# Kernel tuning notes

Measured on AMD Instinct MI355X. Metric: run time of the kernel, lower is better.

Reference implementation:

```python
import jax, jax.numpy as jnp
import numpy as np

B, C, ROWS, COLS = 16, 1, 128, 128
E, H, L, VOCAB = 64, 32, 3, 258


def setup_inputs() -> dict:
    key = jax.random.key(0)
    ks = jax.random.split(key, 18)
    s = 0.05
    d = {
        "x": jax.random.randint(ks[0], (B, C, ROWS, COLS), 0, VOCAB, dtype=jnp.int32),
        "embed_table": jax.random.normal(ks[1], (VOCAB, E), jnp.float32) * s,
    }
    in_sizes = [E + 1, H, H]
    k = 2
    for l in range(L):
        d[f"w_ih_l{l}"] = jax.random.normal(ks[k], (3 * H, in_sizes[l]), jnp.float32) * s; k += 1
        d[f"w_hh_l{l}"] = jax.random.normal(ks[k], (3 * H, H), jnp.float32) * s; k += 1
        d[f"b_ih_l{l}"] = jax.random.normal(ks[k], (3 * H,), jnp.float32) * s; k += 1
        d[f"b_hh_l{l}"] = jax.random.normal(ks[k], (3 * H,), jnp.float32) * s; k += 1
    d["w_h2e"] = jax.random.normal(ks[14], (E + 1, H), jnp.float32) * s
    d["b_h2e"] = jax.random.normal(ks[15], (E + 1,), jnp.float32) * s
    d["w_out"] = jax.random.normal(ks[16], (VOCAB, H), jnp.float32) * s
    d["b_out"] = jax.random.normal(ks[17], (VOCAB,), jnp.float32) * s
    return d


def _forward(x, embed_table, wih, whh, bih, bhh, w_h2e, b_h2e, w_out, b_out):
    b, c, rows, cols = x.shape
    T = cols * c  # GRU sequence length per row
    Hh = whh[0].shape[1]
    nL = len(wih)

    xf = x.reshape(b, rows, T)
    emb = embed_table[xf]  # [B, rows, T, E]
    # normalized row coordinate in [-1, 1), appended as extra feature
    row_pos = jnp.arange(rows, dtype=emb.dtype) / rows * 2.0 - 1.0
    row_feat = jnp.broadcast_to(row_pos[None, :, None, None], (b, rows, T, 1))
    xin = jnp.concatenate([emb, row_feat], axis=-1)  # [B, rows, T, E+1]

    def gru_step(h, x_t):
        # h: [L, B, H]; x_t: [B, E+1]. torch GRU gate order: r, z, n.
        inp = x_t
        hs = []
        for l in range(nL):
            gi = inp @ wih[l].T + bih[l]
            gh = h[l] @ whh[l].T + bhh[l]
            ir, iz, inn = jnp.split(gi, 3, axis=-1)
            hr, hz, hn = jnp.split(gh, 3, axis=-1)
            r = jax.nn.sigmoid(ir + hr)
            z = jax.nn.sigmoid(iz + hz)
            n = jnp.tanh(inn + r * hn)
            hl = (1.0 - z) * n + z * h[l]
            hs.append(hl)
            inp = hl
        return jnp.stack(hs), inp  # emit top-layer output

    def row_step(prev_out, x_row):
        # prev_out: [B, T, H] top-layer GRU output of previous row
        comb = x_row + prev_out @ w_h2e.T + b_h2e  # [B, T, E+1]
        h0 = jnp.zeros((nL, b, Hh), comb.dtype)  # fresh h0 per row, as in torch
        _, out = jax.lax.scan(gru_step, h0, jnp.swapaxes(comb, 0, 1))  # [T, B, H]
        out = jnp.swapaxes(out, 0, 1)  # [B, T, H]
        return out, out

    prev0 = jnp.zeros((b, T, Hh), xin.dtype)
    _, outs = jax.lax.scan(row_step, prev0, jnp.swapaxes(xin, 0, 1))  # [rows, B, T, H]
    outs = jnp.swapaxes(outs, 0, 1)  # [B, rows, T, H]
    pred = outs @ w_out.T + b_out  # [B, rows, T, 258]
    return pred.reshape(b, c, rows, cols, VOCAB)


def reference(x, embed_table, w_ih_l0, w_hh_l0, b_ih_l0, b_hh_l0,
              w_ih_l1, w_hh_l1, b_ih_l1, b_hh_l1,
              w_ih_l2, w_hh_l2, b_ih_l2, b_hh_l2,
              w_h2e, b_h2e, w_out, b_out):
    return _forward(x, embed_table,
                    (w_ih_l0, w_ih_l1, w_ih_l2),
                    (w_hh_l0, w_hh_l1, w_hh_l2),
                    (b_ih_l0, b_ih_l1, b_ih_l2),
                    (b_hh_l0, b_hh_l1, b_hh_l2),
                    w_h2e, b_h2e, w_out, b_out)
```

## Files before the change

kernel.cpp:

```cpp
#include <hip/hip_runtime.h>
#include <math.h>

#define BATCH 16
#define RWS   128
#define TT    128
#define HH    32
#define GG    96
#define RPB   8
#define NRG   (RWS/RPB)
#define WP    100
#define FSTR  16

#define H2_BYTES   (BATCH*RWS*TT*HH*4)
#define FLAG_OFF   H2_BYTES
#define FLAG_BYTES (NRG*BATCH*FSTR*4)
#define PTAB_OFF   (FLAG_OFF + FLAG_BYTES)
#define WF_OFF     (PTAB_OFF + 258*GG*4)

__device__ __forceinline__ float sigm(float x) { return 1.0f / (1.0f + __expf(-x)); }
__device__ __forceinline__ float tanhfast(float x) {
  x = fminf(fmaxf(x, -15.0f), 15.0f);
  float e = __expf(2.0f * x);
  return (e - 1.0f) / (e + 1.0f);
}

__device__ __forceinline__ void barrier_lgkm() {
  __builtin_amdgcn_sched_barrier(0);
  asm volatile("s_waitcnt lgkmcnt(0)" ::: "memory");
  __builtin_amdgcn_s_barrier();
  __builtin_amdgcn_sched_barrier(0);
}

__device__ __forceinline__ float dot32p(const float4* __restrict__ w, const float4 v[8]) {
  float a0 = 0.f, a1 = 0.f, a2 = 0.f, a3 = 0.f;
#pragma unroll
  for (int c = 0; c < 8; ++c) {
    float4 W = w[c];
    a0 = fmaf(W.x, v[c].x, a0);
    a1 = fmaf(W.y, v[c].y, a1);
    a2 = fmaf(W.z, v[c].z, a2);
    a3 = fmaf(W.w, v[c].w, a3);
  }
  return (a0 + a1) + (a2 + a3);
}

__device__ __forceinline__ void hoist8(float4 dst[8], const float* __restrict__ src) {
  const float4* p = (const float4*)src;
#pragma unroll
  for (int c = 0; c < 8; ++c) dst[c] = p[c];
}

__global__ __launch_bounds__(128)
void prep_kernel(const float* __restrict__ emb, const float* __restrict__ wih0,
                 const float* __restrict__ bih0, const float* __restrict__ wh2e,
                 const float* __restrict__ bh2e, float* __restrict__ Ptab,
                 float* __restrict__ Wfo) {
  const int blk = blockIdx.x, tid = threadIdx.x;
  if (blk < 258) {
    if (tid < GG) {
      const float* wr = wih0 + tid * 65;
      const float* e  = emb + blk * 64;
      float acc = bih0[tid];
      for (int k = 0; k < 64; ++k) acc = fmaf(wr[k], e[k], acc);
      for (int k = 0; k < 65; ++k) acc = fmaf(wr[k], bh2e[k], acc);
      Ptab[blk * GG + tid] = acc;
    }
  } else {
    const int g = blk - 258;
    if (tid < HH) {
      const float* wr = wih0 + g * 65;
      float acc = 0.f;
      for (int k = 0; k < 65; ++k) acc = fmaf(wr[k], wh2e[k * HH + tid], acc);
      Wfo[g * HH + tid] = acc;
    }
  }
}

__device__ __forceinline__ void loadmat_packed(const float* __restrict__ src,
                                               float* __restrict__ dst, int tid) {
  for (int i = tid; i < GG * HH; i += 256) {
    const int g = i >> 5, k = i & 31;
    const int gate = g >> 5, j = g & 31;
    dst[j * WP + gate * 32 + k] = src[g * 32 + k];
  }
}

__global__ __launch_bounds__(256, 1)
void rnn_kernel(const int* __restrict__ xg, const float* __restrict__ wih0,
                const float* __restrict__ whh0g, const float* __restrict__ bhh0g,
                const float* __restrict__ wih1g, const float* __restrict__ whh1g,
                const float* __restrict__ bih1g, const float* __restrict__ bhh1g,
                const float* __restrict__ wih2g, const float* __restrict__ whh2g,
                const float* __restrict__ bih2g, const float* __restrict__ bhh2g,
                const float* __restrict__ Ptab, const float* __restrict__ Wfg,
                float* __restrict__ h2buf, int* __restrict__ flags) {
  extern __shared__ __align__(16) float lds[];
  float* Wf    = lds;
  float* Whh0  = Wf   + HH * WP;
  float* Wih1  = Whh0 + HH * WP;
  float* Whh1  = Wih1 + HH * WP;
  float* Wih2  = Whh1 + HH * WP;
  float* Whh2  = Wih2 + HH * WP;
  float* prevs = Whh2 + HH * WP;
  float* h0s   = prevs + HH;
  float* h1s   = h0s + RPB * HH;
  float* h2a   = h1s + RPB * HH;
  float* h2b   = h2a + RPB * HH;

  const int tid = threadIdx.x;
  const int j   = tid & 31;
  const int s   = tid >> 5;
  const int g   = blockIdx.x >> 4;
  const int bat = blockIdx.x & 15;
  const int row = g * RPB + s;

  loadmat_packed(Wfg,   Wf,   tid);
  loadmat_packed(whh0g, Whh0, tid);
  loadmat_packed(wih1g, Wih1, tid);
  loadmat_packed(whh1g, Whh1, tid);
  loadmat_packed(wih2g, Wih2, tid);
  loadmat_packed(whh2g, Whh2, tid);
  h0s[tid] = 0.f; h1s[tid] = 0.f; h2a[tid] = 0.f; h2b[tid] = 0.f;
  if (tid < HH) prevs[tid] = 0.f;

  const float bh0r = bhh0g[j], bh0z = bhh0g[32 + j], bh0n = bhh0g[64 + j];
  const float bi1r = bih1g[j], bi1z = bih1g[32 + j], bi1n = bih1g[64 + j];
  const float bh1r = bhh1g[j], bh1z = bhh1g[32 + j], bh1n = bhh1g[64 + j];
  const float bi2r = bih2g[j], bi2z = bih2g[32 + j], bi2n = bih2g[64 + j];
  const float bh2r_ = bhh2g[j], bh2z_ = bhh2g[32 + j], bh2n_ = bhh2g[64 + j];
  const float rowpos = (float)row * (2.0f / 128.0f) - 1.0f;
  const float rpr = wih0[j * 65 + 64] * rowpos;
  const float rpz = wih0[(32 + j) * 65 + 64] * rowpos;
  const float rpn = wih0[(64 + j) * 65 + 64] * rowpos;
  __syncthreads();

  float h0r = 0.f, h1r = 0.f, h2r = 0.f;
  float4 Vh0[8], Vh1[8], Vh2[8], Vp[8];
#pragma unroll
  for (int c = 0; c < 8; ++c) {
    Vh0[c] = make_float4(0.f, 0.f, 0.f, 0.f);
    Vh1[c] = make_float4(0.f, 0.f, 0.f, 0.f);
    Vh2[c] = make_float4(0.f, 0.f, 0.f, 0.f);
  }

  const size_t xbase = (size_t)(bat * RWS + row) * TT;
  const size_t obase = (size_t)(bat * RWS + row) * TT * HH + j;
  const size_t pbase = (row > 0) ? ((size_t)(bat * RWS + (row - 1)) * TT * HH + j) : 0;
  int* myflag = flags + (g * BATCH + bat) * FSTR;
  const int* pflag = flags + ((g > 0 ? g - 1 : 0) * BATCH + bat) * FSTR;

  int vcur = xg[xbase];
  float pvq = 0.f;
  int lastF = 0;

  if (g > 0) {
    if (tid == 0) {
      int f;
      do { f = __hip_atomic_load(pflag, __ATOMIC_RELAXED, __HIP_MEMORY_SCOPE_AGENT); }
      while (f < 1);
      lastF = f;
    }
    __syncthreads();
    if (s == 0)
      pvq = __hip_atomic_load(h2buf + pbase, __ATOMIC_RELAXED, __HIP_MEMORY_SCOPE_AGENT);
  }

  for (int i = 0; i < TT + RPB - 1; ++i) {
    const int t = i - s;
    const bool act = (t >= 0) && (t < TT);
    const float* h2rd = (i & 1) ? h2a : h2b;
    float*       h2w  = (i & 1) ? h2b : h2a;

    if (tid == 224 && i >= RPB) {
      asm volatile("s_waitcnt vmcnt(0)" ::: "memory");
      __hip_atomic_store(myflag, i - (RPB - 1), __ATOMIC_RELAXED, __HIP_MEMORY_SCOPE_AGENT);
    }

    const int tn = t + 1;
    const int vnext = (tn >= 0 && tn < TT) ? xg[xbase + tn] : 0;
    const float Pr = Ptab[vcur * GG + j];
    const float Pz = Ptab[vcur * GG + 32 + j];
    const float Pn = Ptab[vcur * GG + 64 + j];

    if (g > 0 && i < TT - 1) {
      if (tid == 0 && lastF < i + 2) {
        int f;
        do { f = __hip_atomic_load(pflag, __ATOMIC_RELAXED, __HIP_MEMORY_SCOPE_AGENT); }
        while (f < i + 2);
        lastF = f;
      }
    }
    barrier_lgkm();

    if (s == 0 && g > 0) {
      if (act) prevs[j] = pvq;
      if (i + 1 < TT)
        pvq = __hip_atomic_load(h2buf + pbase + (size_t)(i + 1) * HH,
                                __ATOMIC_RELAXED, __HIP_MEMORY_SCOPE_AGENT);
    }

    if (act) {
      const float ghr0 = bh0r + dot32p((const float4*)(Whh0 + j * WP),      Vh0);
      const float ghz0 = bh0z + dot32p((const float4*)(Whh0 + j * WP + 32), Vh0);
      const float ghn0 = bh0n + dot32p((const float4*)(Whh0 + j * WP + 64), Vh0);
      const float ghr1 = bh1r + dot32p((const float4*)(Whh1 + j * WP),      Vh1);
      const float ghz1 = bh1z + dot32p((const float4*)(Whh1 + j * WP + 32), Vh1);
      const float ghn1 = bh1n + dot32p((const float4*)(Whh1 + j * WP + 64), Vh1);
      const float ghr2 = bh2r_ + dot32p((const float4*)(Whh2 + j * WP),      Vh2);
      const float ghz2 = bh2z_ + dot32p((const float4*)(Whh2 + j * WP + 32), Vh2);
      const float ghn2 = bh2n_ + dot32p((const float4*)(Whh2 + j * WP + 64), Vh2);

      hoist8(Vp, (s == 0) ? prevs : (h2rd + (s - 1) * HH));
      {
        const float gir = Pr + rpr + dot32p((const float4*)(Wf + j * WP),      Vp);
        const float giz = Pz + rpz + dot32p((const float4*)(Wf + j * WP + 32), Vp);
        const float gin = Pn + rpn + dot32p((const float4*)(Wf + j * WP + 64), Vp);
        const float rg = sigm(gir + ghr0);
        const float zg = sigm(giz + ghz0);
        const float ng = tanhfast(gin + rg * ghn0);
        h0r = (1.f - zg) * ng + zg * h0r;
      }
      h0s[s * HH + j] = h0r;
      hoist8(Vh0, h0s + s * HH);

      {
        const float gir = bi1r + dot32p((const float4*)(Wih1 + j * WP),      Vh0);
        const float giz = bi1z + dot32p((const float4*)(Wih1 + j * WP + 32), Vh0);
        const float gin = bi1n + dot32p((const float4*)(Wih1 + j * WP + 64), Vh0);
        const float rg = sigm(gir + ghr1);
        const float zg = sigm(giz + ghz1);
        const float ng = tanhfast(gin + rg * ghn1);
        h1r = (1.f - zg) * ng + zg * h1r;
      }
      h1s[s * HH + j] = h1r;
      hoist8(Vh1, h1s + s * HH);

      {
        const float gir = bi2r + dot32p((const float4*)(Wih2 + j * WP),      Vh1);
        const float giz = bi2z + dot32p((const float4*)(Wih2 + j * WP + 32), Vh1);
        const float gin = bi2n + dot32p((const float4*)(Wih2 + j * WP + 64), Vh1);
        const float rg = sigm(gir + ghr2);
        const float zg = sigm(giz + ghz2);
        const float ng = tanhfast(gin + rg * ghn2);
        h2r = (1.f - zg) * ng + zg * h2r;
      }
      h2w[s * HH + j] = h2r;
      hoist8(Vh2, h2w + s * HH);

      if (s == RPB - 1) {
        __hip_atomic_store(h2buf + obase + (size_t)t * HH, h2r,
                           __ATOMIC_RELAXED, __HIP_MEMORY_SCOPE_AGENT);
      } else {
        h2buf[obase + (size_t)t * HH] = h2r;
      }
    }

    vcur = vnext;
  }

  if (tid == 224) {
    asm volatile("s_waitcnt vmcnt(0)" ::: "memory");
    __hip_atomic_store(myflag, TT, __ATOMIC_RELAXED, __HIP_MEMORY_SCOPE_AGENT);
  }
}

__global__ __launch_bounds__(256)
void proj_kernel(const float* __restrict__ h2buf, const float* __restrict__ wout,
                 const float* __restrict__ bout, float* __restrict__ out) {
  __shared__ float stage[32 * 258];
  const int tid = threadIdx.x;
  const int p = tid & 31, vq = tid >> 5;
  const size_t pos = (size_t)blockIdx.x * 32 + p;
  const float* hrow = h2buf + pos * HH;
  float h[HH];
#pragma unroll
  for (int k = 0; k < HH; k += 4) {
    float4 f = *(const float4*)(hrow + k);
    h[k] = f.x; h[k + 1] = f.y; h[k + 2] = f.z; h[k + 3] = f.w;
  }
#pragma unroll 1
  for (int vi = 0; vi <= 32; ++vi) {
    int v = vq + vi * 8;
    if (v < 258) {
      const float* wrow = wout + v * HH;
      float a0 = bout[v], a1 = 0.f;
#pragma unroll
      for (int k = 0; k < HH; k += 4) {
        float4 w = *(const float4*)(wrow + k);
        a0 = fmaf(w.x, h[k],     fmaf(w.y, h[k + 1], a0));
        a1 = fmaf(w.z, h[k + 2], fmaf(w.w, h[k + 3], a1));
      }
      stage[p * 258 + v] = a0 + a1;
    }
  }
  __syncthreads();
  float* o = out + (size_t)blockIdx.x * 32 * 258;
#pragma unroll 1
  for (int i = tid; i < 32 * 258; i += 256) o[i] = stage[i];
}

extern "C" void kernel_launch(void* const* d_in, const int* in_sizes, int n_in,
                              void* d_out, int out_size, void* d_ws, size_t ws_size,
                              hipStream_t stream) {
  const int*   x    = (const int*)d_in[0];
  const float* emb  = (const float*)d_in[1];
  const float* wih0 = (const float*)d_in[2];
  const float* whh0 = (const float*)d_in[3];
  const float* bih0 = (const float*)d_in[4];
  const float* bhh0 = (const float*)d_in[5];
  const float* wih1 = (const float*)d_in[6];
  const float* whh1 = (const float*)d_in[7];
  const float* bih1 = (const float*)d_in[8];
  const float* bhh1 = (const float*)d_in[9];
  const float* wih2 = (const float*)d_in[10];
  const float* whh2 = (const float*)d_in[11];
  const float* bih2 = (const float*)d_in[12];
  const float* bhh2 = (const float*)d_in[13];
  const float* wh2e = (const float*)d_in[14];
  const float* bh2e = (const float*)d_in[15];
  const float* wout = (const float*)d_in[16];
  const float* bout = (const float*)d_in[17];
  float* out = (float*)d_out;

  char*  ws    = (char*)d_ws;
  float* h2buf = (float*)ws;
  int*   flags = (int*)(ws + FLAG_OFF);
  float* Ptab  = (float*)(ws + PTAB_OFF);
  float* Wf    = (float*)(ws + WF_OFF);

  hipMemsetAsync(flags, 0, FLAG_BYTES, stream);
  prep_kernel<<<354, 128, 0, stream>>>(emb, wih0, bih0, wh2e, bh2e, Ptab, Wf);

  const int rnn_lds_bytes = (6 * HH * WP + HH + 4 * RPB * HH) * 4;
  hipFuncSetAttribute((const void*)rnn_kernel,
                      hipFuncAttributeMaxDynamicSharedMemorySize, rnn_lds_bytes);
  rnn_kernel<<<NRG * BATCH, 256, rnn_lds_bytes, stream>>>(
      x, wih0, whh0, bhh0, wih1, whh1, bih1, bhh1, wih2, whh2, bih2, bhh2,
      Ptab, Wf, h2buf, flags);

  proj_kernel<<<8192, 256, 0, stream>>>(h2buf, wout, bout, out);
}
```

Baseline: 1.678 ms.

## Keep two recurrent weight matrices in registers and compute hidden gates eagerly

Moves the layer-0 and layer-2 hidden-to-hidden weights out of LDS into per-thread registers (192 VGPRs' worth) and shrinks the LDS footprint. Each layer's recurrent gate preactivations are now computed right after its new hidden state is produced and carried into the next step, so the separate per-layer hidden vectors (Vh0/Vh1/Vh2) collapse into one temporary. It also inserts s_sleep into the inter-block flag spin-waits to reduce polling pressure. The aim is fewer LDS reads per step and less register pressure from held vectors, at the risk of high VGPR use or spills from the register-resident weights.

```diff
diff --git a/kernel.cpp b/kernel.cpp
--- a/kernel.cpp
+++ b/kernel.cpp
@@ -40,6 +40,18 @@
     a1 = fmaf(W.y, v[c].y, a1);
     a2 = fmaf(W.z, v[c].z, a2);
     a3 = fmaf(W.w, v[c].w, a3);
+  }
+  return (a0 + a1) + (a2 + a3);
+}
+
+__device__ __forceinline__ float dotrr(const float4 w[8], const float4 v[8]) {
+  float a0 = 0.f, a1 = 0.f, a2 = 0.f, a3 = 0.f;
+#pragma unroll
+  for (int c = 0; c < 8; ++c) {
+    a0 = fmaf(w[c].x, v[c].x, a0);
+    a1 = fmaf(w[c].y, v[c].y, a1);
+    a2 = fmaf(w[c].z, v[c].z, a2);
+    a3 = fmaf(w[c].w, v[c].w, a3);
   }
   return (a0 + a1) + (a2 + a3);
 }
@@ -96,12 +108,10 @@
                 float* __restrict__ h2buf, int* __restrict__ flags) {
   extern __shared__ __align__(16) float lds[];
   float* Wf    = lds;
-  float* Whh0  = Wf   + HH * WP;
-  float* Wih1  = Whh0 + HH * WP;
+  float* Wih1  = Wf   + HH * WP;
   float* Whh1  = Wih1 + HH * WP;
   float* Wih2  = Whh1 + HH * WP;
-  float* Whh2  = Wih2 + HH * WP;
-  float* prevs = Whh2 + HH * WP;
+  float* prevs = Wih2 + HH * WP;
   float* h0s   = prevs + HH;
   float* h1s   = h0s + RPB * HH;
   float* h2a   = h1s + RPB * HH;
@@ -115,13 +125,26 @@
   const int row = g * RPB + s;
 
   loadmat_packed(Wfg,   Wf,   tid);
-  loadmat_packed(whh0g, Whh0, tid);
   loadmat_packed(wih1g, Wih1, tid);
   loadmat_packed(whh1g, Whh1, tid);
   loadmat_packed(wih2g, Wih2, tid);
-  loadmat_packed(whh2g, Whh2, tid);
   h0s[tid] = 0.f; h1s[tid] = 0.f; h2a[tid] = 0.f; h2b[tid] = 0.f;
   if (tid < HH) prevs[tid] = 0.f;
+
+  float4 Wh0r[8], Wh0z[8], Wh0n[8], Wh2r[8], Wh2z[8], Wh2n[8];
+  {
+    const float4* W0 = (const float4*)whh0g;
+    const float4* W2 = (const float4*)whh2g;
+#pragma unroll
+    for (int c = 0; c < 8; ++c) {
+      Wh0r[c] = W0[j * 8 + c];
+      Wh0z[c] = W0[(32 + j) * 8 + c];
+      Wh0n[c] = W0[(64 + j) * 8 + c];
+      Wh2r[c] = W2[j * 8 + c];
+      Wh2z[c] = W2[(32 + j) * 8 + c];
+      Wh2n[c] = W2[(64 + j) * 8 + c];
+    }
+  }
 
   const float bh0r = bhh0g[j], bh0z = bhh0g[32 + j], bh0n = bhh0g[64 + j];
   const float bi1r = bih1g[j], bi1z = bih1g[32 + j], bi1n = bih1g[64 + j];
@@ -135,13 +158,9 @@
   __syncthreads();
 
   float h0r = 0.f, h1r = 0.f, h2r = 0.f;
-  float4 Vh0[8], Vh1[8], Vh2[8], Vp[8];
-#pragma unroll
-  for (int c = 0; c < 8; ++c) {
-    Vh0[c] = make_float4(0.f, 0.f, 0.f, 0.f);
-    Vh1[c] = make_float4(0.f, 0.f, 0.f, 0.f);
-    Vh2[c] = make_float4(0.f, 0.f, 0.f, 0.f);
-  }
+  float ghr0p = bh0r, ghz0p = bh0z, ghn0p = bh0n;
+  float ghr1p = bh1r, ghz1p = bh1z, ghn1p = bh1n;
+  float ghr2p = bh2r_, ghz2p = bh2z_, ghn2p = bh2n_;
 
   const size_t xbase = (size_t)(bat * RWS + row) * TT;
   const size_t obase = (size_t)(bat * RWS + row) * TT * HH + j;
@@ -157,7 +176,7 @@
     if (tid == 0) {
       int f;
       do { f = __hip_atomic_load(pflag, __ATOMIC_RELAXED, __HIP_MEMORY_SCOPE_AGENT); }
-      while (f < 1);
+      while (f < 1 ? (__builtin_amdgcn_s_sleep(1), true) : false);
       lastF = f;
     }
     __syncthreads();
@@ -185,8 +204,10 @@
     if (g > 0 && i < TT - 1) {
       if (tid == 0 && lastF < i + 2) {
         int f;
-        do { f = __hip_atomic_load(pflag, __ATOMIC_RELAXED, __HIP_MEMORY_SCOPE_AGENT); }
-        while (f < i + 2);
+        do {
+          f = __hip_atomic_load(pflag, __ATOMIC_RELAXED, __HIP_MEMORY_SCOPE_AGENT);
+          if (f < i + 2) __builtin_amdgcn_s_sleep(1);
+        } while (f < i + 2);
         lastF = f;
       }
     }
@@ -200,52 +221,53 @@
     }
 
     if (act) {
-      const float ghr0 = bh0r + dot32p((const float4*)(Whh0 + j * WP),      Vh0);
-      const float ghz0 = bh0z + dot32p((const float4*)(Whh0 + j * WP + 32), Vh0);
-      const float ghn0 = bh0n + dot32p((const float4*)(Whh0 + j * WP + 64), Vh0);
-      const float ghr1 = bh1r + dot32p((const float4*)(Whh1 + j * WP),      Vh1);
-      const float ghz1 = bh1z + dot32p((const float4*)(Whh1 + j * WP + 32), Vh1);
-      const float ghn1 = bh1n + dot32p((const float4*)(Whh1 + j * WP + 64), Vh1);
-      const float ghr2 = bh2r_ + dot32p((const float4*)(Whh2 + j * WP),      Vh2);
-      const float ghz2 = bh2z_ + dot32p((const float4*)(Whh2 + j * WP + 32), Vh2);
-      const float ghn2 = bh2n_ + dot32p((const float4*)(Whh2 + j * WP + 64), Vh2);
-
-      hoist8(Vp, (s == 0) ? prevs : (h2rd + (s - 1) * HH));
+      float4 Vt[8];
+
+      hoist8(Vt, (s == 0) ? prevs : (h2rd + (s - 1) * HH));
       {
-        const float gir = Pr + rpr + dot32p((const float4*)(Wf + j * WP),      Vp);
-        const float giz = Pz + rpz + dot32p((const float4*)(Wf + j * WP + 32), Vp);
-        const float gin = Pn + rpn + dot32p((const float4*)(Wf + j * WP + 64), Vp);
-        const float rg = sigm(gir + ghr0);
-        const float zg = sigm(giz + ghz0);
-        const float ng = tanhfast(gin + rg * ghn0);
+        const float gir = Pr + rpr + dot32p((const float4*)(Wf + j * WP),      Vt);
+        const float giz = Pz + rpz + dot32p((const float4*)(Wf + j * WP + 32), Vt);
+        const float gin = Pn + rpn + dot32p((const float4*)(Wf + j * WP + 64), Vt);
+        const float rg = sigm(gir + ghr0p);
+        const float zg = sigm(giz + ghz0p);
+        const float ng = tanhfast(gin + rg * ghn0p);
         h0r = (1.f - zg) * ng + zg * h0r;
       }
       h0s[s * HH + j] = h0r;
-      hoist8(Vh0, h0s + s * HH);
+      hoist8(Vt, h0s + s * HH);
 
       {
-        const float gir = bi1r + dot32p((const float4*)(Wih1 + j * WP),      Vh0);
-        const float giz = bi1z + dot32p((const float4*)(Wih1 + j * WP + 32), Vh0);
-        const float gin = bi1n + dot32p((const float4*)(Wih1 + j * WP + 64), Vh0);
-        const float rg = sigm(gir + ghr1);
-        const float zg = sigm(giz + ghz1);
-        const float ng = tanhfast(gin + rg * ghn1);
+        const float gir = bi1r + dot32p((const float4*)(Wih1 + j * WP),      Vt);
+        const float giz = bi1z + dot32p((const float4*)(Wih1 + j * WP + 32), Vt);
+        const float gin = bi1n + dot32p((const float4*)(Wih1 + j * WP + 64), Vt);
+        ghr0p = bh0r + dotrr(Wh0r, Vt);
+        ghz0p = bh0z + dotrr(Wh0z, Vt);
+        ghn0p = bh0n + dotrr(Wh0n, Vt);
+        const float rg = sigm(gir + ghr1p);
+        const float zg = sigm(giz + ghz1p);
+        const float ng = tanhfast(gin + rg * ghn1p);
         h1r = (1.f - zg) * ng + zg * h1r;
       }
       h1s[s * HH + j] = h1r;
-      hoist8(Vh1, h1s + s * HH);
+      hoist8(Vt, h1s + s * HH);
 
       {
-        const float gir = bi2r + dot32p((const float4*)(Wih2 + j * WP),      Vh1);
-        const float giz = bi2z + dot32p((const float4*)(Wih2 + j * WP + 32), Vh1);
-        const float gin = bi2n + dot32p((const float4*)(Wih2 + j * WP + 64), Vh1);
-        const float rg = sigm(gir + ghr2);
-        const float zg = sigm(giz + ghz2);
-        const float ng = tanhfast(gin + rg * ghn2);
+        const float gir = bi2r + dot32p((const float4*)(Wih2 + j * WP),      Vt);
+        const float giz = bi2z + dot32p((const float4*)(Wih2 + j * WP + 32), Vt);
+        const float gin = bi2n + dot32p((const float4*)(Wih2 + j * WP + 64), Vt);
+        ghr1p = bh1r + dot32p((const float4*)(Whh1 + j * WP),      Vt);
+        ghz1p = bh1z + dot32p((const float4*)(Whh1 + j * WP + 32), Vt);
+        ghn1p = bh1n + dot32p((const float4*)(Whh1 + j * WP + 64), Vt);
+        const float rg = sigm(gir + ghr2p);
+        const float zg = sigm(giz + ghz2p);
+        const float ng = tanhfast(gin + rg * ghn2p);
         h2r = (1.f - zg) * ng + zg * h2r;
       }
       h2w[s * HH + j] = h2r;
-      hoist8(Vh2, h2w + s * HH);
+      hoist8(Vt, h2w + s * HH);
+      ghr2p = bh2r_ + dotrr(Wh2r, Vt);
+      ghz2p = bh2z_ + dotrr(Wh2z, Vt);
+      ghn2p = bh2n_ + dotrr(Wh2n, Vt);
 
       if (s == RPB - 1) {
         __hip_atomic_store(h2buf + obase + (size_t)t * HH, h2r,
@@ -331,7 +353,7 @@
   hipMemsetAsync(flags, 0, FLAG_BYTES, stream);
   prep_kernel<<<354, 128, 0, stream>>>(emb, wih0, bih0, wh2e, bh2e, Ptab, Wf);
 
-  const int rnn_lds_bytes = (6 * HH * WP + HH + 4 * RPB * HH) * 4;
+  const int rnn_lds_bytes = (4 * HH * WP + HH + 4 * RPB * HH) * 4;
   hipFuncSetAttribute((const void*)rnn_kernel,
                       hipFuncAttributeMaxDynamicSharedMemorySize, rnn_lds_bytes);
   rnn_kernel<<<NRG * BATCH, 256, rnn_lds_bytes, stream>>>(
```

Result: faster. 1.624 ms (-3.2%).
